# Performance work log

Measured on AMD Instinct MI355X. Metric: run time of the kernel, lower is better.

Reference implementation:

```python
import jax, jax.numpy as jnp
import numpy as np

N_POINTS = 100000
K_VOL = 27          # 3^3 hypercube kernel offsets
PAIRS = 60000       # active in/out pairs per kernel offset
C_IN = 64
C_OUT = 64


def setup_inputs() -> dict:
    key = jax.random.key(0)
    k1, k2, k3, k4, k5 = jax.random.split(key, 5)
    stdv = 1.0 / np.sqrt(C_IN * K_VOL)  # matches reset_parameters
    inputs = {
        "input": jax.random.normal(k1, (N_POINTS, C_IN), dtype=jnp.float32),
        "kernel": jax.random.uniform(k2, (K_VOL, C_IN, C_OUT), dtype=jnp.float32,
                                      minval=-stdv, maxval=stdv),
        "bias": jax.random.uniform(k3, (1, C_OUT), dtype=jnp.float32,
                                    minval=-stdv, maxval=stdv),
        # per-offset kernel maps (normally produced from coordinate hashing in metadata)
        "in_map": jax.random.randint(k4, (K_VOL, PAIRS), 0, N_POINTS, dtype=jnp.int32),
        "out_map": jax.random.randint(k5, (K_VOL, PAIRS), 0, N_POINTS, dtype=jnp.int32),
    }
    return inputs


def reference(input, kernel, bias, in_map, out_map):
    # Sparse convolution: for each kernel offset k, gather input rows via
    # in_map[k], apply the per-offset GEMM with kernel[k], and scatter-add
    # the results into the output rows given by out_map[k].
    K, P = in_map.shape
    n_out = input.shape[0]
    gathered = input[in_map]                         # [K, P, Cin]  (gather)
    per_offset = jnp.einsum('kpi,kio->kpo', gathered, kernel)  # [K, P, Cout] (GEMM)
    out = jax.ops.segment_sum(per_offset.reshape(K * P, -1),
                              out_map.reshape(-1),
                              num_segments=n_out)    # [N, Cout] (scatter-add)
    return out + bias
```

## Files before the change

### kernel.cpp

```cpp
#include <hip/hip_runtime.h>
#include <hip/hip_bf16.h>

#define N_POINTS 100000
#define K_VOL 27
#define PAIRS 60000
#define CCH 64
#define TILES_PER_K (PAIRS / 16)
#define BX 64
#define NWAVES 4

#define RPB 64
#define NBUCKETS ((N_POINTS + RPB - 1) / RPB)
#define NBINS (NBUCKETS * K_VOL)
#define CAP 96
#define SENT 0xFFFFFFFFu
#define CNTSTRIDE 32

#define PREP_BLKS 6250
#define FILL_BLKS (K_VOL * 64)
#define PSUB (PAIRS / 8)

#define WS_ENT 0
#define WS_CNT (NBINS * CAP * 4)
#define WS_INBF (WS_CNT + NBUCKETS * CNTSTRIDE * 4)
#define WS_WT (WS_INBF + N_POINTS * CCH * 2)
#define WS_NEED (WS_WT + K_VOL * CCH * CCH * 2)

typedef __bf16 bf16x8 __attribute__((ext_vector_type(8)));
typedef __bf16 bf16x4 __attribute__((ext_vector_type(4)));
typedef float f32x4 __attribute__((ext_vector_type(4)));


__global__ __launch_bounds__(256) void prep_fill_kernel(
    const float* __restrict__ input, const float* __restrict__ weight,
    const int* __restrict__ in_map, const int* __restrict__ out_map,
    unsigned char* __restrict__ ws) {
  const int bid = blockIdx.x;
  if (bid < PREP_BLKS) {
    int t = bid * 256 + threadIdx.x;
    float4 v = ((const float4*)input)[t];
    bf16x4 o;
    o[0] = (__bf16)v.x; o[1] = (__bf16)v.y; o[2] = (__bf16)v.z; o[3] = (__bf16)v.w;
    *(bf16x4*)(ws + WS_INBF + (size_t)t * 8) = o;
    if (t < K_VOL * CCH * CCH) {
      int k = t >> 12;
      int r = t & 4095;
      int ci = r >> 6, co = r & 63;
      *(__bf16*)(ws + WS_WT + (size_t)(((k * 64 + co) << 6) + ci) * 2) =
          (__bf16)weight[t];
    }
  } else {
    const int f = bid - PREP_BLKS;
    const int k = f >> 6;
    const int bx = f & 63;
    const int slice = bx & 7;
    const int sub = bx >> 3;
    const int pbeg = sub * PSUB, pend = pbeg + PSUB;
    const int* omp_ = out_map + k * PAIRS;
    const int* imp_ = in_map + k * PAIRS;
    unsigned int* cntp = (unsigned int*)(ws + WS_CNT);
    unsigned int* entp = (unsigned int*)(ws + WS_ENT);
    for (int p = pbeg + (int)threadIdx.x * 4; p < pend; p += 1024) {
      int4 om4 = *(const int4*)(omp_ + p);
      int4 im4 = *(const int4*)(imp_ + p);
      int oms[4] = {om4.x, om4.y, om4.z, om4.w};
      int ims[4] = {im4.x, im4.y, im4.z, im4.w};
#pragma unroll
      for (int j = 0; j < 4; ++j) {
        int bkt = oms[j] >> 6;
        if ((bkt & 7) != slice) continue;
        unsigned int pos = atomicAdd(cntp + (bkt << 5) + k, 1u);
        if (pos < CAP)
          entp[(bkt * K_VOL + k) * CAP + pos] =
              (unsigned int)ims[j] | ((unsigned int)(oms[j] & 63) << 17);
      }
    }
  }
}

__global__ __launch_bounds__(256) void spconv_main_kernel(
    const float* __restrict__ bias, const unsigned char* __restrict__ ws,
    float* __restrict__ out) {
  __shared__ __align__(16) unsigned char lds[4 * 8192];
  const unsigned int* cnt = (const unsigned int*)(ws + WS_CNT);
  const unsigned int* entries = (const unsigned int*)(ws + WS_ENT);
  const __bf16* inbf = (const __bf16*)(ws + WS_INBF);
  const __bf16* wt = (const __bf16*)(ws + WS_WT);

  const int b = blockIdx.x;
  const int tid = threadIdx.x;
  const int wave = tid >> 6, lane = tid & 63;
  const int c = lane & 15, q = lane >> 4;
  unsigned char* stage = lds + wave * 8192;
  unsigned char* pmat = stage + 4096;

#pragma unroll
  for (int i = 0; i < 16; ++i)
    *(float*)(pmat + i * 256 + lane * 4) = 0.f;

  f32x4 acc[4][4];
#pragma unroll
  for (int rb = 0; rb < 4; ++rb)
#pragma unroll
    for (int nt = 0; nt < 4; ++nt) acc[rb][nt] = (f32x4){0.f, 0.f, 0.f, 0.f};

  bf16x8 bfA0[4], bfA1[4];

  auto grow = [&](unsigned v, bf16x8& x0, bf16x8& x1) {
    unsigned r = (v == SENT) ? 0u : (v & 0x1FFFFu);
    const __bf16* ar = inbf + ((size_t)r << 6);
    x0 = *(const bf16x8*)(ar + q * 8);
    x1 = *(const bf16x8*)(ar + 32 + q * 8);
  };

  auto do_tile = [&](unsigned entL, unsigned entH, bf16x8 aL0, bf16x8 aL1,
                     bf16x8 aH0, bf16x8 aH1) {
    int mol0 = -1, mol1 = -1;
    if (q == 0 && entL != SENT) mol0 = (int)(entL >> 17);
    if (q == 1 && entH != SENT) mol1 = (int)(entH >> 17);
    if (mol0 >= 0) {
      int m = c;
      *(__bf16*)(pmat + mol0 * 64 + (((m >> 3) ^ (mol0 & 3)) << 4) + (m & 7) * 2) =
          (__bf16)1.0f;
    }
    if (mol1 >= 0) {
      int m = 16 + c;
      *(__bf16*)(pmat + mol1 * 64 + (((m >> 3) ^ (mol1 & 3)) << 4) + (m & 7) * 2) =
          (__bf16)1.0f;
    }

    f32x4 c1a[4], c1b[4];
#pragma unroll
    for (int nt = 0; nt < 4; ++nt) {
      c1a[nt] = (f32x4){0.f, 0.f, 0.f, 0.f};
      c1b[nt] = (f32x4){0.f, 0.f, 0.f, 0.f};
    }
#pragma unroll
    for (int nt = 0; nt < 4; ++nt) {
      c1a[nt] = __builtin_amdgcn_mfma_f32_16x16x32_bf16(aL0, bfA0[nt], c1a[nt],
                                                        0, 0, 0);
      c1a[nt] = __builtin_amdgcn_mfma_f32_16x16x32_bf16(aL1, bfA1[nt], c1a[nt],
                                                        0, 0, 0);
      c1b[nt] = __builtin_amdgcn_mfma_f32_16x16x32_bf16(aH0, bfA0[nt], c1b[nt],
                                                        0, 0, 0);
      c1b[nt] = __builtin_amdgcn_mfma_f32_16x16x32_bf16(aH1, bfA1[nt], c1b[nt],
                                                        0, 0, 0);
    }

#pragma unroll
    for (int nt = 0; nt < 4; ++nt) {
      const int n = nt * 16 + c;
      const int swz = n & 3;
      const int in0 = (q & 1) * 8;
      bf16x4 h0, h1;
#pragma unroll
      for (int r = 0; r < 4; ++r) {
        h0[r] = (__bf16)c1a[nt][r];
        h1[r] = (__bf16)c1b[nt][r];
      }
      *(bf16x4*)(stage + n * 64 + (((q >> 1) ^ swz) << 4) + in0) = h0;
      *(bf16x4*)(stage + n * 64 + (((2 + (q >> 1)) ^ swz) << 4) + in0) = h1;
    }

    bf16x8 pfrag[4];
#pragma unroll
    for (int rb = 0; rb < 4; ++rb)
      pfrag[rb] = *(const bf16x8*)(pmat + (rb * 16 + c) * 64 + ((q ^ (c & 3)) << 4));
#pragma unroll
    for (int nt = 0; nt < 4; ++nt) {
      const int n = nt * 16 + c;
      const bf16x8 bb = *(const bf16x8*)(stage + n * 64 + ((q ^ (n & 3)) << 4));
#pragma unroll
      for (int rb = 0; rb < 4; ++rb)
        acc[rb][nt] = __builtin_amdgcn_mfma_f32_16x16x32_bf16(pfrag[rb], bb,
                                                             acc[rb][nt], 0, 0, 0);
    }

    if (mol0 >= 0) {
      int m = c;
      *(__bf16*)(pmat + mol0 * 64 + (((m >> 3) ^ (mol0 & 3)) << 4) + (m & 7) * 2) =
          (__bf16)0.0f;
    }
    if (mol1 >= 0) {
      int m = 16 + c;
      *(__bf16*)(pmat + mol1 * 64 + (((m >> 3) ^ (mol1 & 3)) << 4) + (m & 7) * 2) =
          (__bf16)0.0f;
    }
  };

  int j = wave;
  unsigned ecp, v0, v1, v2, v3;
  bf16x8 pa00, pa01, pa10, pa11, pa20, pa21, pa30, pa31;
  {
    unsigned cn = cnt[(b << 5) + j];
    const unsigned* bp = entries + (size_t)(b * K_VOL + j) * CAP;
    unsigned g0 = bp[c], g1 = bp[16 + c], g2 = bp[32 + c], g3 = bp[48 + c];
    ecp = cn > CAP ? (unsigned)CAP : cn;
    v0 = ((unsigned)c < ecp) ? g0 : SENT;
    v1 = ((unsigned)(16 + c) < ecp) ? g1 : SENT;
    v2 = ((unsigned)(32 + c) < ecp) ? g2 : SENT;
    v3 = ((unsigned)(48 + c) < ecp) ? g3 : SENT;
    grow(v0, pa00, pa01); grow(v1, pa10, pa11);
    grow(v2, pa20, pa21); grow(v3, pa30, pa31);
  }
#pragma unroll
  for (int nt = 0; nt < 4; ++nt) {
    const __bf16* wrow = wt + ((j * 64 + nt * 16 + c) << 6);
    bfA0[nt] = *(const bf16x8*)(wrow + q * 8);
    bfA1[nt] = *(const bf16x8*)(wrow + 32 + q * 8);
  }

  while (j < K_VOL) {
    const int jn = j + 4;
    const bool hasn = jn < K_VOL;
    const unsigned ec = ecp;
    const unsigned w0 = v0, w1 = v1, w2 = v2, w3 = v3;
    const bf16x8 qa00 = pa00, qa01 = pa01, qa10 = pa10, qa11 = pa11;
    const bf16x8 qa20 = pa20, qa21 = pa21, qa30 = pa30, qa31 = pa31;

    unsigned ncn = 0, g0 = SENT, g1 = SENT, g2 = SENT, g3 = SENT;
    if (hasn) {
      ncn = cnt[(b << 5) + jn];
      const unsigned* bpn = entries + (size_t)(b * K_VOL + jn) * CAP;
      g0 = bpn[c]; g1 = bpn[16 + c]; g2 = bpn[32 + c]; g3 = bpn[48 + c];
    }

    if (ec) do_tile(w0, w1, qa00, qa01, qa10, qa11);

    if (hasn) {
      ecp = ncn > CAP ? (unsigned)CAP : ncn;
      v0 = ((unsigned)c < ecp) ? g0 : SENT;
      v1 = ((unsigned)(16 + c) < ecp) ? g1 : SENT;
      v2 = ((unsigned)(32 + c) < ecp) ? g2 : SENT;
      v3 = ((unsigned)(48 + c) < ecp) ? g3 : SENT;
      grow(v0, pa00, pa01); grow(v1, pa10, pa11);
      grow(v2, pa20, pa21); grow(v3, pa30, pa31);
    }

    if (ec > 32) do_tile(w2, w3, qa20, qa21, qa30, qa31);

    for (unsigned tb = 64; tb < ec; tb += 32) {
      const unsigned* base = entries + (size_t)(b * K_VOL + j) * CAP;
      unsigned i0 = tb + c, i1 = tb + 16 + c;
      unsigned e0 = (i0 < ec) ? base[i0] : SENT;
      unsigned e1 = (i1 < ec) ? base[i1] : SENT;
      bf16x8 x00, x01, x10, x11;
      grow(e0, x00, x01);
      grow(e1, x10, x11);
      do_tile(e0, e1, x00, x01, x10, x11);
    }

    if (hasn) {
#pragma unroll
      for (int nt = 0; nt < 4; ++nt) {
        const __bf16* wrow = wt + ((jn * 64 + nt * 16 + c) << 6);
        bfA0[nt] = *(const bf16x8*)(wrow + q * 8);
        bfA1[nt] = *(const bf16x8*)(wrow + 32 + q * 8);
      }
    }
    j = jn;
  }

  __syncthreads();
  float* bufA = (float*)lds;
  float* bufB = (float*)(lds + 16384);

  auto REDST = [&](float* buf) {
#pragma unroll
    for (int rb = 0; rb < 4; ++rb)
#pragma unroll
      for (int nt = 0; nt < 4; ++nt)
#pragma unroll
        for (int r = 0; r < 4; ++r) {
          int row = rb * 16 + q * 4 + r;
          int col = (nt * 16 + c) ^ (q << 2) ^ ((q & 1) << 4);
          buf[row * 64 + col] = acc[rb][nt][r];
        }
  };
  auto REDADD = [&](const float* buf) {
#pragma unroll
    for (int rb = 0; rb < 4; ++rb)
#pragma unroll
      for (int nt = 0; nt < 4; ++nt)
#pragma unroll
        for (int r = 0; r < 4; ++r) {
          int row = rb * 16 + q * 4 + r;
          int col = (nt * 16 + c) ^ (q << 2) ^ ((q & 1) << 4);
          acc[rb][nt][r] += buf[row * 64 + col];
        }
  };

  if (wave == 1) REDST(bufA);
  if (wave == 3) REDST(bufB);
  __syncthreads();
  if (wave == 0) REDADD(bufA);
  if (wave == 2) REDADD(bufB);
  __syncthreads();
  if (wave == 2) REDST(bufA);
  __syncthreads();
  if (wave == 0) {
    REDADD(bufA);
    float bv[4];
#pragma unroll
    for (int nt = 0; nt < 4; ++nt) bv[nt] = bias[nt * 16 + c];
#pragma unroll
    for (int rb = 0; rb < 4; ++rb)
#pragma unroll
      for (int r = 0; r < 4; ++r) {
        const int row = b * RPB + rb * 16 + q * 4 + r;
        if (row < N_POINTS) {
#pragma unroll
          for (int nt = 0; nt < 4; ++nt)
            out[row * CCH + nt * 16 + c] = acc[rb][nt][r] + bv[nt];
        }
      }
  }
}


__global__ __launch_bounds__(256) void init_out_kernel(
    const float* __restrict__ bias, float* __restrict__ out) {
  int tid = blockIdx.x * blockDim.x + threadIdx.x;
  int c4 = tid & 15;
  float4 b = ((const float4*)bias)[c4];
  ((float4*)out)[tid] = b;
}

__global__ __launch_bounds__(256) void spconv_kernel(
    const float* __restrict__ input, const float* __restrict__ weight,
    const int* __restrict__ in_map, const int* __restrict__ out_map,
    float* __restrict__ out) {
  const int k = blockIdx.y;
  const int lane = threadIdx.x & 63;
  const int wave = threadIdx.x >> 6;
  const int col = lane & 15;
  const int quad = lane >> 4;

  const float* Wk = weight + k * (CCH * CCH);
  bf16x8 bfrag[4][2];
#pragma unroll
  for (int nt = 0; nt < 4; ++nt) {
    int co = nt * 16 + col;
#pragma unroll
    for (int s = 0; s < 2; ++s) {
      int ci0 = s * 32 + quad * 8;
      bf16x8 f;
#pragma unroll
      for (int j = 0; j < 8; ++j) f[j] = (__bf16)Wk[(ci0 + j) * CCH + co];
      bfrag[nt][s] = f;
    }
  }

  const int* im = in_map + k * PAIRS;
  const int* om = out_map + k * PAIRS;

  for (int tile = blockIdx.x * NWAVES + wave; tile < TILES_PER_K;
       tile += BX * NWAVES) {
    const int pbase = tile * 16;
    int rin = im[pbase + col];
    const float* arow = input + rin * CCH;
    bf16x8 afrag[2];
#pragma unroll
    for (int s = 0; s < 2; ++s) {
      const float4 x0 = *(const float4*)(arow + s * 32 + quad * 8);
      const float4 x1 = *(const float4*)(arow + s * 32 + quad * 8 + 4);
      bf16x8 f;
      f[0] = (__bf16)x0.x; f[1] = (__bf16)x0.y;
      f[2] = (__bf16)x0.z; f[3] = (__bf16)x0.w;
      f[4] = (__bf16)x1.x; f[5] = (__bf16)x1.y;
      f[6] = (__bf16)x1.z; f[7] = (__bf16)x1.w;
      afrag[s] = f;
    }

    f32x4 acc[4];
#pragma unroll
    for (int nt = 0; nt < 4; ++nt) acc[nt] = (f32x4){0.f, 0.f, 0.f, 0.f};
#pragma unroll
    for (int nt = 0; nt < 4; ++nt) {
      acc[nt] = __builtin_amdgcn_mfma_f32_16x16x32_bf16(afrag[0], bfrag[nt][0],
                                                        acc[nt], 0, 0, 0);
      acc[nt] = __builtin_amdgcn_mfma_f32_16x16x32_bf16(afrag[1], bfrag[nt][1],
                                                        acc[nt], 0, 0, 0);
    }

    int orow[4];
#pragma unroll
    for (int r = 0; r < 4; ++r) orow[r] = om[pbase + quad * 4 + r];
#pragma unroll
    for (int r = 0; r < 4; ++r) {
      float* op = out + orow[r] * CCH + col;
#pragma unroll
      for (int nt = 0; nt < 4; ++nt) atomicAdd(op + nt * 16, acc[nt][r]);
    }
  }
}


extern "C" void kernel_launch(void* const* d_in, const int* in_sizes, int n_in,
                              void* d_out, int out_size, void* d_ws,
                              size_t ws_size, hipStream_t stream) {
  const float* input = (const float*)d_in[0];
  const float* weight = (const float*)d_in[1];
  const float* bias = (const float*)d_in[2];
  const int* in_map = (const int*)d_in[3];
  const int* out_map = (const int*)d_in[4];
  float* out = (float*)d_out;

  if (d_ws != nullptr && ws_size >= (size_t)WS_NEED) {
    unsigned char* ws = (unsigned char*)d_ws;
    hipMemsetAsync(ws + WS_CNT, 0, NBUCKETS * CNTSTRIDE * 4, stream);
    prep_fill_kernel<<<PREP_BLKS + FILL_BLKS, 256, 0, stream>>>(
        input, weight, in_map, out_map, ws);
    spconv_main_kernel<<<NBUCKETS, 256, 0, stream>>>(bias, ws, out);
  } else {
    init_out_kernel<<<(N_POINTS * 16) / 256, 256, 0, stream>>>(bias, out);
    dim3 grid(BX, K_VOL);
    spconv_kernel<<<grid, 256, 0, stream>>>(input, weight, in_map, out_map, out);
  }
}
```

Baseline: 265.7 us.

## Aggregate bucket counters in LDS and deepen entry prefetch pipeline

The fill phase now counts bucket hits per block in shared memory, reserves each bucket's range with one global atomic, and then assigns slots through LDS atomics. This replaces one global atomic per pair with one per bucket per block, at the cost of reading out_map twice. In the main kernel, entry indices are prefetched two offsets ahead and the gathered rows one offset ahead, so index-load latency is hidden deeper. That pipelining adds register pressure.

```diff
diff --git a/kernel.cpp b/kernel.cpp
--- a/kernel.cpp
+++ b/kernel.cpp
@@ -19,6 +19,7 @@
 #define PREP_BLKS 6250
 #define FILL_BLKS (K_VOL * 64)
 #define PSUB (PAIRS / 8)
+#define NLB 200
 
 #define WS_ENT 0
 #define WS_CNT (NBINS * CAP * 4)
@@ -50,6 +51,8 @@
           (__bf16)weight[t];
     }
   } else {
+    __shared__ unsigned int lcnt[NLB];
+    __shared__ unsigned int lcur[NLB];
     const int f = bid - PREP_BLKS;
     const int k = f >> 6;
     const int bx = f & 63;
@@ -60,6 +63,30 @@
     const int* imp_ = in_map + k * PAIRS;
     unsigned int* cntp = (unsigned int*)(ws + WS_CNT);
     unsigned int* entp = (unsigned int*)(ws + WS_ENT);
+
+    for (int i = threadIdx.x; i < NLB; i += 256) lcnt[i] = 0;
+    __syncthreads();
+
+    for (int p = pbeg + (int)threadIdx.x * 4; p < pend; p += 1024) {
+      int4 om4 = *(const int4*)(omp_ + p);
+      int oms[4] = {om4.x, om4.y, om4.z, om4.w};
+#pragma unroll
+      for (int j = 0; j < 4; ++j) {
+        int bkt = oms[j] >> 6;
+        if ((bkt & 7) == slice) atomicAdd(&lcnt[bkt >> 3], 1u);
+      }
+    }
+    __syncthreads();
+
+    for (int lb = threadIdx.x; lb < NLB; lb += 256) {
+      unsigned n = lcnt[lb];
+      if (n) {
+        int bkt = (lb << 3) | slice;
+        lcur[lb] = atomicAdd(cntp + (bkt << 5) + k, n);
+      }
+    }
+    __syncthreads();
+
     for (int p = pbeg + (int)threadIdx.x * 4; p < pend; p += 1024) {
       int4 om4 = *(const int4*)(omp_ + p);
       int4 im4 = *(const int4*)(imp_ + p);
@@ -69,10 +96,10 @@
       for (int j = 0; j < 4; ++j) {
         int bkt = oms[j] >> 6;
         if ((bkt & 7) != slice) continue;
-        unsigned int pos = atomicAdd(cntp + (bkt << 5) + k, 1u);
+        unsigned pos = atomicAdd(&lcur[bkt >> 3], 1u);
         if (pos < CAP)
           entp[(bkt * K_VOL + k) * CAP + pos] =
-              (unsigned int)ims[j] | ((unsigned int)(oms[j] & 63) << 17);
+              (unsigned)ims[j] | ((unsigned)(oms[j] & 63) << 17);
       }
     }
   }
@@ -189,19 +216,31 @@
   };
 
   int j = wave;
-  unsigned ecp, v0, v1, v2, v3;
-  bf16x8 pa00, pa01, pa10, pa11, pa20, pa21, pa30, pa31;
+  unsigned ec, w0, w1, w2, w3;
+  bf16x8 qa00, qa01, qa10, qa11, qa20, qa21, qa30, qa31;
+  unsigned ecn, x0, x1, x2, x3;
   {
-    unsigned cn = cnt[(b << 5) + j];
-    const unsigned* bp = entries + (size_t)(b * K_VOL + j) * CAP;
-    unsigned g0 = bp[c], g1 = bp[16 + c], g2 = bp[32 + c], g3 = bp[48 + c];
-    ecp = cn > CAP ? (unsigned)CAP : cn;
-    v0 = ((unsigned)c < ecp) ? g0 : SENT;
-    v1 = ((unsigned)(16 + c) < ecp) ? g1 : SENT;
-    v2 = ((unsigned)(32 + c) < ecp) ? g2 : SENT;
-    v3 = ((unsigned)(48 + c) < ecp) ? g3 : SENT;
-    grow(v0, pa00, pa01); grow(v1, pa10, pa11);
-    grow(v2, pa20, pa21); grow(v3, pa30, pa31);
+    unsigned cn0 = cnt[(b << 5) + j];
+    const unsigned* bp0 = entries + (size_t)(b * K_VOL + j) * CAP;
+    unsigned a0 = bp0[c], a1 = bp0[16 + c], a2 = bp0[32 + c], a3 = bp0[48 + c];
+    unsigned cn1 = 0, b0 = SENT, b1 = SENT, b2 = SENT, b3 = SENT;
+    if (j + 4 < K_VOL) {
+      cn1 = cnt[(b << 5) + j + 4];
+      const unsigned* bp1 = entries + (size_t)(b * K_VOL + j + 4) * CAP;
+      b0 = bp1[c]; b1 = bp1[16 + c]; b2 = bp1[32 + c]; b3 = bp1[48 + c];
+    }
+    ec = cn0 > CAP ? (unsigned)CAP : cn0;
+    w0 = ((unsigned)c < ec) ? a0 : SENT;
+    w1 = ((unsigned)(16 + c) < ec) ? a1 : SENT;
+    w2 = ((unsigned)(32 + c) < ec) ? a2 : SENT;
+    w3 = ((unsigned)(48 + c) < ec) ? a3 : SENT;
+    grow(w0, qa00, qa01); grow(w1, qa10, qa11);
+    grow(w2, qa20, qa21); grow(w3, qa30, qa31);
+    ecn = cn1 > CAP ? (unsigned)CAP : cn1;
+    x0 = ((unsigned)c < ecn) ? b0 : SENT;
+    x1 = ((unsigned)(16 + c) < ecn) ? b1 : SENT;
+    x2 = ((unsigned)(32 + c) < ecn) ? b2 : SENT;
+    x3 = ((unsigned)(48 + c) < ecn) ? b3 : SENT;
   }
 #pragma unroll
   for (int nt = 0; nt < 4; ++nt) {
@@ -211,43 +250,33 @@
   }
 
   while (j < K_VOL) {
-    const int jn = j + 4;
-    const bool hasn = jn < K_VOL;
-    const unsigned ec = ecp;
-    const unsigned w0 = v0, w1 = v1, w2 = v2, w3 = v3;
-    const bf16x8 qa00 = pa00, qa01 = pa01, qa10 = pa10, qa11 = pa11;
-    const bf16x8 qa20 = pa20, qa21 = pa21, qa30 = pa30, qa31 = pa31;
-
-    unsigned ncn = 0, g0 = SENT, g1 = SENT, g2 = SENT, g3 = SENT;
+    const int jn = j + 4, jf = j + 8;
+    const bool hasn = jn < K_VOL, hasf = jf < K_VOL;
+
+    bf16x8 pa00, pa01, pa10, pa11, pa20, pa21, pa30, pa31;
     if (hasn) {
-      ncn = cnt[(b << 5) + jn];
-      const unsigned* bpn = entries + (size_t)(b * K_VOL + jn) * CAP;
-      g0 = bpn[c]; g1 = bpn[16 + c]; g2 = bpn[32 + c]; g3 = bpn[48 + c];
+      grow(x0, pa00, pa01); grow(x1, pa10, pa11);
+      grow(x2, pa20, pa21); grow(x3, pa30, pa31);
+    }
+
+    unsigned fc = 0, h0 = SENT, h1 = SENT, h2 = SENT, h3 = SENT;
+    if (hasf) {
+      fc = cnt[(b << 5) + jf];
+      const unsigned* bpf = entries + (size_t)(b * K_VOL + jf) * CAP;
+      h0 = bpf[c]; h1 = bpf[16 + c]; h2 = bpf[32 + c]; h3 = bpf[48 + c];
     }
 
     if (ec) do_tile(w0, w1, qa00, qa01, qa10, qa11);
-
-    if (hasn) {
-      ecp = ncn > CAP ? (unsigned)CAP : ncn;
-      v0 = ((unsigned)c < ecp) ? g0 : SENT;
-      v1 = ((unsigned)(16 + c) < ecp) ? g1 : SENT;
-      v2 = ((unsigned)(32 + c) < ecp) ? g2 : SENT;
-      v3 = ((unsigned)(48 + c) < ecp) ? g3 : SENT;
-      grow(v0, pa00, pa01); grow(v1, pa10, pa11);
-      grow(v2, pa20, pa21); grow(v3, pa30, pa31);
-    }
-
     if (ec > 32) do_tile(w2, w3, qa20, qa21, qa30, qa31);
-
     for (unsigned tb = 64; tb < ec; tb += 32) {
       const unsigned* base = entries + (size_t)(b * K_VOL + j) * CAP;
       unsigned i0 = tb + c, i1 = tb + 16 + c;
       unsigned e0 = (i0 < ec) ? base[i0] : SENT;
       unsigned e1 = (i1 < ec) ? base[i1] : SENT;
-      bf16x8 x00, x01, x10, x11;
-      grow(e0, x00, x01);
-      grow(e1, x10, x11);
-      do_tile(e0, e1, x00, x01, x10, x11);
+      bf16x8 y00, y01, y10, y11;
+      grow(e0, y00, y01);
+      grow(e1, y10, y11);
+      do_tile(e0, e1, y00, y01, y10, y11);
     }
 
     if (hasn) {
@@ -258,6 +287,16 @@
         bfA1[nt] = *(const bf16x8*)(wrow + 32 + q * 8);
       }
     }
+
+    ec = ecn;
+    w0 = x0; w1 = x1; w2 = x2; w3 = x3;
+    qa00 = pa00; qa01 = pa01; qa10 = pa10; qa11 = pa11;
+    qa20 = pa20; qa21 = pa21; qa30 = pa30; qa31 = pa31;
+    ecn = fc > CAP ? (unsigned)CAP : fc;
+    x0 = ((unsigned)c < ecn) ? h0 : SENT;
+    x1 = ((unsigned)(16 + c) < ecn) ? h1 : SENT;
+    x2 = ((unsigned)(32 + c) < ecn) ? h2 : SENT;
+    x3 = ((unsigned)(48 + c) < ecn) ? h3 : SENT;
     j = jn;
   }
 
```

After: 227.2 us. 14.5% less time.
